# Kernel optimization log

Measured on AMD Instinct MI355X. Metric: run time of the kernel, lower is better.

The kernel has to match this reference:

```python
import jax, jax.numpy as jnp
import numpy as np

N, E, IN_DIM, HID = 100000, 1600000, 128, 256
AA_DIM, POS_DIM, MAX_POS = 64, 32, 512


def setup_inputs() -> dict:
    key = jax.random.key(0)
    ks = jax.random.split(key, 16)
    x = jax.random.normal(ks[0], (N, IN_DIM), dtype=jnp.float32)
    edge_index = jax.random.randint(ks[1], (2, E), 0, N, dtype=jnp.int64)
    edge_weight = jax.random.uniform(ks[2], (E,), dtype=jnp.float32)
    mut_mask = jnp.zeros((N,), dtype=jnp.float32).at[123].set(1.0)  # one-hot mutation site
    wt_idx = jax.random.randint(ks[3], (1,), 0, 20, dtype=jnp.int64)
    mut_idx = jax.random.randint(ks[4], (1,), 0, 20, dtype=jnp.int64)
    def glorot(k, shape):
        fan = shape[0] + shape[1]
        return jax.random.uniform(k, shape, jnp.float32, -1.0, 1.0) * np.sqrt(6.0 / fan)
    W1 = glorot(ks[5], (IN_DIM, HID)); b1 = jnp.zeros((HID,), jnp.float32)
    W2 = glorot(ks[6], (HID, HID));    b2 = jnp.zeros((HID,), jnp.float32)
    aa_emb = jax.random.normal(ks[7], (20, AA_DIM), dtype=jnp.float32)
    pos_emb = jax.random.normal(ks[8], (MAX_POS, POS_DIM), dtype=jnp.float32)
    FEAT = HID + AA_DIM * 3 + POS_DIM  # 480
    Wh1 = glorot(ks[9], (FEAT, 512));  bh1 = jnp.zeros((512,), jnp.float32)
    Wh2 = glorot(ks[10], (512, 128));  bh2 = jnp.zeros((128,), jnp.float32)
    Wh3 = glorot(ks[11], (128, 1));    bh3 = jnp.zeros((1,), jnp.float32)
    return dict(x=x, edge_index=edge_index, edge_weight=edge_weight, mut_mask=mut_mask,
                wt_idx=wt_idx, mut_idx=mut_idx, W1=W1, b1=b1, W2=W2, b2=b2,
                aa_emb=aa_emb, pos_emb=pos_emb, Wh1=Wh1, bh1=bh1, Wh2=Wh2, bh2=bh2,
                Wh3=Wh3, bh3=bh3)


def _gcn_conv(x, W, b, row, col, ew, n):
    # PyG GCNConv: h = x W; out[col] += norm * h[row]; norm = d^-1/2[row]*ew*d^-1/2[col]
    deg = jax.ops.segment_sum(ew, col, num_segments=n)
    dinv = jnp.where(deg > 0, jax.lax.rsqrt(jnp.maximum(deg, 1e-12)), 0.0)
    norm = dinv[row] * ew * dinv[col]
    h = x @ W
    out = jax.ops.segment_sum(h[row] * norm[:, None], col, num_segments=n)
    return out + b


def reference(x, edge_index, edge_weight, mut_mask, wt_idx, mut_idx,
              W1, b1, W2, b2, aa_emb, pos_emb, Wh1, bh1, Wh2, bh2, Wh3, bh3):
    n = x.shape[0]
    # add self loops with weight 1 (GCNConv default, fill_value=1.0)
    loop = jnp.arange(n, dtype=edge_index.dtype)
    row = jnp.concatenate([edge_index[0], loop])
    col = jnp.concatenate([edge_index[1], loop])
    ew = jnp.concatenate([edge_weight, jnp.ones((n,), edge_weight.dtype)])
    # encode (dropout is identity in eval mode)
    h = jax.nn.relu(_gcn_conv(x, W1, b1, row, col, ew, n))
    h = jax.nn.relu(_gcn_conv(h, W2, b2, row, col, ew, n))
    # masked sum -> [1, HID]
    z = (h * mut_mask[:, None]).sum(axis=0, keepdims=True)
    wt = aa_emb[wt_idx.reshape(-1)]
    mut = aa_emb[mut_idx.reshape(-1)]
    delta = mut - wt
    pos = jnp.clip(jnp.argmax(mut_mask), 0, pos_emb.shape[0] - 1).reshape(1)
    pe = pos_emb[pos]
    feat = jnp.concatenate([z, wt, mut, delta, pe], axis=1)  # [1, 480]
    f = jax.nn.relu(feat @ Wh1 + bh1)
    f = jax.nn.relu(f @ Wh2 + bh2)
    out = f @ Wh3 + bh3  # [1, 1]
    return out[0, 0]
```

## Files before the change

### kernel.cpp

```cpp
#include <hip/hip_runtime.h>


#define SCAP   512
#define L1CAP  512
#define L2CAP  16384
#define HID    256
#define INDIM  128
#define HSZ    4096
#define BITW   4096
#define NSCAN  2048
#define NB     1024
#define NTB    32

struct WsPtrs {
  int* cnt;
  float* deg;
  int* hash;
  int* l1r; float* l1w;
  int* l2r; int* l2s; float* l2w;
  int* wscol;
  float* h2;
  float* C;
  float* f2pre;
};

__global__ void kinit(WsPtrs w, const int* eiraw, const float* mask, int N, int E) {
  int g = blockIdx.x * blockDim.x + threadIdx.x;
  int gs = gridDim.x * blockDim.x;
  for (int j = g; j < N; j += gs)
    if (mask[j] > 0.f) w.cnt[4] = j;
  for (int j = g; j < HSZ; j += gs) w.hash[j] = -1;
  if (g < HID) w.h2[g] = 0.f;
  if (g < 128) w.f2pre[g] = 0.f;
  if (g < 3) w.cnt[g] = 0;
  if (g >= 8 && g < 16) w.cnt[g] = 0;
  if (g == 3) {
    int bad = 0;
    long step = E / 20; if (step < 1) step = 1;
    #pragma unroll
    for (int j = 1; j <= 16; ++j) {
      long idx = (long)j * step;
      if (idx < E) bad |= (eiraw[2 * idx + 1] != 0);
    }
    w.cnt[3] = bad ? 0 : 1;
  }
}

__device__ __forceinline__ void hins(WsPtrs& w, int u) {
  unsigned h = ((unsigned)u * 2654435761u) >> 20;
  for (;;) {
    int cur = __hip_atomic_load(&w.hash[h], __ATOMIC_RELAXED, __HIP_MEMORY_SCOPE_AGENT);
    if (cur == u) return;
    if (cur == -1) {
      int old = atomicCAS(&w.hash[h], -1, u);
      if (old == -1) { w.deg[u] = 1.0f; return; }
      if (old == u) return;
    }
    h = (h + 1) & (HSZ - 1);
  }
}

__device__ __forceinline__ void join(int* ctr, int tid, int target) {
  __threadfence();
  __syncthreads();
  if (tid == 0) {
    __hip_atomic_fetch_add(ctr, 1, __ATOMIC_RELEASE, __HIP_MEMORY_SCOPE_AGENT);
    while (__hip_atomic_load(ctr, __ATOMIC_ACQUIRE, __HIP_MEMORY_SCOPE_AGENT) < target)
      __builtin_amdgcn_s_sleep(4);
  }
  __syncthreads();
}

__device__ __forceinline__ float warmf4(const float* base, int nf4, int tid) {
  const float4* p = (const float4*)base;
  float a = 0.f;
  for (int i = tid; i < nf4; i += 256) { float4 v = p[i]; a += v.x + v.y + v.z + v.w; }
  return a;
}

__device__ __forceinline__ int dedup_s1(WsPtrs& w, int n1, int* l1rS, float* l1wS,
                                        int* s1sL, int* nsS, int tid) {
  for (int i = tid; i < n1; i += 256) { l1rS[i] = w.l1r[i]; l1wS[i] = w.l1w[i]; }
  __syncthreads();
  if (tid == 0) {
    int ns = 0;
    for (int i = 0; i < n1; ++i) {
      int v = l1rS[i]; bool seen = false;
      for (int j = 0; j < ns; ++j) if (s1sL[j] == v) { seen = true; break; }
      if (!seen && ns < SCAP) s1sL[ns++] = v;
    }
    *nsS = ns;
  }
  __syncthreads();
  return *nsS;
}

__global__ void kpassA(WsPtrs w, const int* eiraw, const float* ew,
                       const int* wtI_, const int* mutI_,
                       const float* aa, const float* pemb, const float* Wh1,
                       const float* W1, const float* W2, const float* Wh2, int E) {
  if (blockIdx.x >= NSCAN + 8) {
    int b8 = blockIdx.x - (NSCAN + 8);
    int tid = threadIdx.x;
    float wa = warmf4(W1  + b8 * 4096, 1024, tid)
             + warmf4(W2  + b8 * 8192, 2048, tid)
             + warmf4(Wh1 + b8 * 16384, 4096, tid)
             + warmf4(Wh2 + b8 * 8192, 2048, tid);
    if (wa == 1.2345e38f) w.cnt[15] = 1;
    return;
  }
  if (blockIdx.x >= NSCAN) {
    __shared__ float fe[224];
    __shared__ float red[256];
    int b8 = blockIdx.x - NSCAN;
    int t = threadIdx.x;
    int wtI = wtI_[0], mutI = mutI_[0];
    if (t < 64) {
      float a = aa[wtI * 64 + t], b = aa[mutI * 64 + t];
      fe[t] = a; fe[64 + t] = b; fe[128 + t] = b - a;
    }
    int tgt = w.cnt[4];
    int pos = tgt > 511 ? 511 : tgt;
    if (t < 32) fe[192 + t] = pemb[pos * 32 + t];
    __syncthreads();
    int o = b8 * 64 + (t & 63), js = t >> 6;
    float v = 0.f;
    for (int j = js * 56; j < js * 56 + 56; ++j)
      v += fe[j] * Wh1[(256 + j) * 512 + o];
    red[t] = v;
    __syncthreads();
    if (t < 64) w.C[b8 * 64 + t] = red[t] + red[64 + t] + red[128 + t] + red[192 + t];
    return;
  }
  const int tgt = w.cnt[4];
  const bool is64 = w.cnt[3] != 0;
  const long long* ell = (const long long*)eiraw;
  int g = blockIdx.x * blockDim.x + threadIdx.x;
  const int gs = NSCAN * 256;
  for (long e = g; e < E; e += gs) {
    int c = is64 ? (int)ell[(long)E + e] : eiraw[(long)E + e];
    w.wscol[e] = c;
    if (c == tgt) {
      int r = is64 ? (int)ell[e] : eiraw[e];
      int i1 = atomicAdd(&w.cnt[0], 1);
      if (i1 < L1CAP) { w.l1r[i1] = r; w.l1w[i1] = ew[e]; }
    }
  }
  if (g == 0) {
    int i1 = atomicAdd(&w.cnt[0], 1);
    if (i1 < L1CAP) { w.l1r[i1] = tgt; w.l1w[i1] = 1.0f; }
  }
}

__global__ void kpassB(WsPtrs w, const int* eiraw, const float* ew, int E) {
  __shared__ int      l1rS[L1CAP];
  __shared__ float    l1wS[L1CAP];
  __shared__ int      s1sL[SCAP];
  __shared__ unsigned bits[BITW];
  __shared__ int      nsS;
  int tid = threadIdx.x;
  const bool is64 = w.cnt[3] != 0;
  const long long* ell = (const long long*)eiraw;
  int n1 = w.cnt[0]; if (n1 > L1CAP) n1 = L1CAP;
  for (int j = tid; j < BITW; j += 256) bits[j] = 0u;
  int ns = dedup_s1(w, n1, l1rS, l1wS, s1sL, &nsS, tid);
  for (int j = tid; j < ns; j += 256) {
    unsigned u = (unsigned)s1sL[j] & (BITW * 32 - 1);
    atomicOr(&bits[u >> 5], 1u << (u & 31));
    if (blockIdx.x == 0) {
      int v = s1sL[j];
      hins(w, v);
      int idx = atomicAdd(&w.cnt[2], 1);
      if (idx < L2CAP) { w.l2r[idx] = v; w.l2s[idx] = j; w.l2w[idx] = 1.0f; }
    }
  }
  __syncthreads();
  int g = blockIdx.x * 256 + tid;
  const int gs = NB * 256;
  const int4* c4 = (const int4*)w.wscol;
  int nv = E >> 2;
  for (int j2 = g; j2 < nv; j2 += gs) {
    int4 vv = c4[j2];
    #pragma unroll
    for (int t = 0; t < 4; ++t) {
      int c = (t == 0) ? vv.x : (t == 1) ? vv.y : (t == 2) ? vv.z : vv.w;
      unsigned u = (unsigned)c & (BITW * 32 - 1);
      if (bits[u >> 5] & (1u << (u & 31))) {
        int s = -1;
        for (int j = 0; j < ns; ++j) if (s1sL[j] == c) { s = j; break; }
        if (s >= 0) {
          long e = 4L * j2 + t;
          int r = is64 ? (int)ell[e] : eiraw[e];
          int idx = atomicAdd(&w.cnt[2], 1);
          if (idx < L2CAP) { w.l2r[idx] = r; w.l2s[idx] = s; w.l2w[idx] = ew[e]; }
          hins(w, r);
        }
      }
    }
  }
  for (long e = 4L * nv + g; e < E; e += gs) {
    int c = w.wscol[e];
    int s = -1;
    for (int j = 0; j < ns; ++j) if (s1sL[j] == c) { s = j; break; }
    if (s >= 0) {
      int r = is64 ? (int)ell[e] : eiraw[e];
      int idx = atomicAdd(&w.cnt[2], 1);
      if (idx < L2CAP) { w.l2r[idx] = r; w.l2s[idx] = s; w.l2w[idx] = ew[e]; }
      hins(w, r);
    }
  }
}

__global__ void kpassC(WsPtrs w, const float* ew, int E) {
  __shared__ unsigned bits[BITW];
  int tid = threadIdx.x;
  for (int j = tid; j < BITW; j += 256) bits[j] = 0u;
  __syncthreads();
  for (int j = tid; j < HSZ; j += 256) {
    int u2 = w.hash[j];
    if (u2 >= 0) {
      unsigned u = (unsigned)u2 & (BITW * 32 - 1);
      atomicOr(&bits[u >> 5], 1u << (u & 31));
    }
  }
  __syncthreads();
  int g = blockIdx.x * 256 + tid;
  const int gs = NB * 256;
  const int4* c4 = (const int4*)w.wscol;
  int nv = E >> 2;
  for (int j2 = g; j2 < nv; j2 += gs) {
    int4 vv = c4[j2];
    #pragma unroll
    for (int t = 0; t < 4; ++t) {
      int c = (t == 0) ? vv.x : (t == 1) ? vv.y : (t == 2) ? vv.z : vv.w;
      unsigned u = (unsigned)c & (BITW * 32 - 1);
      if (bits[u >> 5] & (1u << (u & 31)))
        atomicAdd(&w.deg[c], ew[4L * j2 + t]);
    }
  }
  for (long e = 4L * nv + g; e < E; e += gs) {
    int c = w.wscol[e];
    unsigned u = (unsigned)c & (BITW * 32 - 1);
    if (bits[u >> 5] & (1u << (u & 31))) atomicAdd(&w.deg[c], ew[e]);
  }
}

__global__ void __launch_bounds__(256) ktail(
    WsPtrs w, const float* x, const float* W1, const float* b1,
    const float* W2, const float* b2, const float* mask,
    const float* Wh1, const float* bh1, const float* Wh2, const float* bh2,
    const float* Wh3, const float* bh3, float* out) {
  __shared__ int   l1rS[L1CAP];
  __shared__ float l1wS[L1CAP];
  __shared__ int   s1sL[SCAP];
  __shared__ int   nsS;
  __shared__ float xs[2][INDIM];
  __shared__ float zL[256];
  __shared__ float pp[256];
  __shared__ float f1L[16];

  int tid = threadIdx.x, bid = blockIdx.x;
  const int tgt = w.cnt[4];
  int n1 = w.cnt[0]; if (n1 > L1CAP) n1 = L1CAP;
  int n2 = w.cnt[2]; if (n2 > L2CAP) n2 = L2CAP;
  int ns = dedup_s1(w, n1, l1rS, l1wS, s1sL, &nsS, tid);
  float dti = rsqrtf(w.deg[tgt]);

  int grp = tid >> 7, lane = tid & 127;
  for (int s = bid; s < ns; s += NTB) {
    int v = s1sL[s];
    float dv = w.deg[v], dvi = rsqrtf(dv);
    ((float*)xs)[tid] = 0.f;
    __syncthreads();
    for (int i = grp; i < n2; i += 2) {
      if (w.l2s[i] == s) {
        int r = w.l2r[i];
        float nrm = rsqrtf(w.deg[r]) * w.l2w[i] * dvi;
        xs[grp][lane] += nrm * x[(long)r * INDIM + lane];
      }
    }
    __syncthreads();
    float h = b1[tid];
    #pragma unroll 8
    for (int k = 0; k < INDIM; ++k) h += (xs[0][k] + xs[1][k]) * W1[k * HID + tid];
    float wsum = 0.f;
    for (int i = 0; i < n1; ++i) if (l1rS[i] == v) wsum += l1wS[i];
    atomicAdd(&w.h2[tid], dvi * wsum * dti * fmaxf(h, 0.f));
    __syncthreads();
  }
  join(&w.cnt[8], tid, NTB);

  pp[tid] = __hip_atomic_load(&w.h2[tid], __ATOMIC_RELAXED, __HIP_MEMORY_SCOPE_AGENT);
  __syncthreads();
  {
    float v = b2[tid];
    #pragma unroll 8
    for (int k = 0; k < HID; ++k) v += pp[k] * W2[k * HID + tid];
    zL[tid] = fmaxf(v, 0.f) * mask[tgt];
  }
  __syncthreads();

  {
    int o0 = bid * 16, o = o0 + (tid & 15), ks = tid >> 4;
    float v = 0.f;
    #pragma unroll 4
    for (int k = ks * 16; k < ks * 16 + 16; ++k) v += zL[k] * Wh1[k * 512 + o];
    pp[tid] = v;
    __syncthreads();
    if (tid < 16) {
      float v2 = w.C[o0 + tid] + bh1[o0 + tid];
      for (int s2 = 0; s2 < 16; ++s2) v2 += pp[s2 * 16 + tid];
      f1L[tid] = fmaxf(v2, 0.f);
    }
    __syncthreads();
    if (tid < 128) {
      float v3 = 0.f;
      #pragma unroll
      for (int j = 0; j < 16; ++j) v3 += f1L[j] * Wh2[(o0 + j) * 128 + tid];
      atomicAdd(&w.f2pre[tid], v3);
    }
  }
  __threadfence();
  __syncthreads();
  if (tid == 0)
    __hip_atomic_fetch_add(&w.cnt[9], 1, __ATOMIC_RELEASE, __HIP_MEMORY_SCOPE_AGENT);
  if (bid != 0) return;
  if (tid == 0)
    while (__hip_atomic_load(&w.cnt[9], __ATOMIC_ACQUIRE,
                             __HIP_MEMORY_SCOPE_AGENT) < NTB)
      __builtin_amdgcn_s_sleep(4);
  __syncthreads();

  if (tid < 128)
    pp[tid] = fmaxf(__hip_atomic_load(&w.f2pre[tid], __ATOMIC_RELAXED,
                                      __HIP_MEMORY_SCOPE_AGENT) + bh2[tid], 0.f)
              * Wh3[tid];
  __syncthreads();
  if (tid == 0) {
    float s = bh3[0];
    for (int k = 0; k < 128; ++k) s += pp[k];
    out[0] = s;
  }
}

extern "C" void kernel_launch(void* const* d_in, const int* in_sizes, int n_in,
                              void* d_out, int out_size, void* d_ws, size_t ws_size,
                              hipStream_t stream) {
  const float* x    = (const float*)d_in[0];
  const int*   ei   = (const int*)d_in[1];
  const float* ew   = (const float*)d_in[2];
  const float* mask = (const float*)d_in[3];
  const int*   wtI  = (const int*)d_in[4];
  const int*   mutI = (const int*)d_in[5];
  const float* W1   = (const float*)d_in[6];
  const float* b1   = (const float*)d_in[7];
  const float* W2   = (const float*)d_in[8];
  const float* b2   = (const float*)d_in[9];
  const float* aa   = (const float*)d_in[10];
  const float* pemb = (const float*)d_in[11];
  const float* Wh1  = (const float*)d_in[12];
  const float* bh1  = (const float*)d_in[13];
  const float* Wh2  = (const float*)d_in[14];
  const float* bh2  = (const float*)d_in[15];
  const float* Wh3  = (const float*)d_in[16];
  const float* bh3  = (const float*)d_in[17];
  float* out = (float*)d_out;
  const int N = in_sizes[3];
  const int E = in_sizes[2];

  char* q = (char*)d_ws;
  auto take = [&](size_t bytes) -> char* {
    char* r = q; q += (bytes + 255) & ~(size_t)255; return r;
  };
  WsPtrs w;
  w.cnt   = (int*)take(64);
  w.deg   = (float*)take((size_t)N * 4);
  w.hash  = (int*)take(HSZ * 4);
  w.l1r   = (int*)take(L1CAP * 4);
  w.l1w   = (float*)take(L1CAP * 4);
  w.l2r   = (int*)take(L2CAP * 4);
  w.l2s   = (int*)take(L2CAP * 4);
  w.l2w   = (float*)take(L2CAP * 4);
  w.wscol = (int*)take((size_t)E * 4);
  w.h2    = (float*)take(HID * 4);
  w.C     = (float*)take(512 * 4);
  w.f2pre = (float*)take(128 * 4);

  kinit  <<<64, 256, 0, stream>>>(w, ei, mask, N, E);
  kpassA <<<NSCAN + 16, 256, 0, stream>>>(w, ei, ew, wtI, mutI, aa, pemb, Wh1,
                                          W1, W2, Wh2, E);
  kpassB <<<NB, 256, 0, stream>>>(w, ei, ew, E);
  kpassC <<<NB, 256, 0, stream>>>(w, ew, E);
  ktail  <<<NTB, 256, 0, stream>>>(w, x, W1, b1, W2, b2, mask,
                                   Wh1, bh1, Wh2, bh2, Wh3, bh3, out);
}
```

Measured before the change: 224.3 us.

## Parallelize tail over edges with global atomics and split matvecs across blocks

The tail kernel now accumulates aggregated neighbour features for all 2-hop nodes into a global buffer with atomics, distributing edges across all blocks instead of each block scanning every edge list per node. The W1 projection is then done block-per-output-slice over shared-memory tiles of the sums, and the W2 matvec is split across blocks with extra grid joins. The column scan in pass A is also vectorized to read two indices per load. This adds extra grid-wide barriers, a zero-initialised workspace buffer and many float atomics.

```diff
diff --git a/kernel.cpp b/kernel.cpp
--- a/kernel.cpp
+++ b/kernel.cpp
@@ -19,8 +19,10 @@
   int* l1r; float* l1w;
   int* l2r; int* l2s; float* l2w;
   int* wscol;
+  float* xsum;
   float* h2;
   float* C;
+  float* z;
   float* f2pre;
 };
 
@@ -30,6 +32,8 @@
   for (int j = g; j < N; j += gs)
     if (mask[j] > 0.f) w.cnt[4] = j;
   for (int j = g; j < HSZ; j += gs) w.hash[j] = -1;
+  float4* xz = (float4*)w.xsum;
+  for (int j = g; j < SCAP * INDIM / 4; j += gs) xz[j] = make_float4(0.f, 0.f, 0.f, 0.f);
   if (g < HID) w.h2[g] = 0.f;
   if (g < 128) w.f2pre[g] = 0.f;
   if (g < 3) w.cnt[g] = 0;
@@ -136,14 +140,38 @@
   const bool is64 = w.cnt[3] != 0;
   const long long* ell = (const long long*)eiraw;
   int g = blockIdx.x * blockDim.x + threadIdx.x;
-  const int gs = NSCAN * 256;
-  for (long e = g; e < E; e += gs) {
-    int c = is64 ? (int)ell[(long)E + e] : eiraw[(long)E + e];
-    w.wscol[e] = c;
-    if (c == tgt) {
-      int r = is64 ? (int)ell[e] : eiraw[e];
-      int i1 = atomicAdd(&w.cnt[0], 1);
-      if (i1 < L1CAP) { w.l1r[i1] = r; w.l1w[i1] = ew[e]; }
+  const long gs = (long)NSCAN * 256;
+  auto hit = [&](long e, int r_unused) {
+    int r = is64 ? (int)ell[e] : eiraw[e];
+    int i1 = atomicAdd(&w.cnt[0], 1);
+    if (i1 < L1CAP) { w.l1r[i1] = r; w.l1w[i1] = ew[e]; }
+  };
+  if ((E & 1) == 0) {
+    long half = E >> 1;
+    int2* ws2 = (int2*)w.wscol;
+    if (is64) {
+      const long2* c2 = (const long2*)(ell + E);
+      for (long j = g; j < half; j += gs) {
+        long2 v = c2[j];
+        int c0 = (int)v.x, c1 = (int)v.y;
+        ws2[j] = make_int2(c0, c1);
+        if (c0 == tgt) hit(2 * j, 0);
+        if (c1 == tgt) hit(2 * j + 1, 0);
+      }
+    } else {
+      const int2* c2 = (const int2*)(eiraw + E);
+      for (long j = g; j < half; j += gs) {
+        int2 v = c2[j];
+        ws2[j] = v;
+        if (v.x == tgt) hit(2 * j, 0);
+        if (v.y == tgt) hit(2 * j + 1, 0);
+      }
+    }
+  } else {
+    for (long e = g; e < E; e += gs) {
+      int c = is64 ? (int)ell[(long)E + e] : eiraw[(long)E + e];
+      w.wscol[e] = c;
+      if (c == tgt) hit(e, 0);
     }
   }
   if (g == 0) {
@@ -254,9 +282,9 @@
   __shared__ float l1wS[L1CAP];
   __shared__ int   s1sL[SCAP];
   __shared__ int   nsS;
-  __shared__ float xs[2][INDIM];
-  __shared__ float zL[256];
-  __shared__ float pp[256];
+  __shared__ float xsL[64 * 129];
+  __shared__ float red[256];
+  __shared__ float vecS[256];
   __shared__ float f1L[16];
 
   int tid = threadIdx.x, bid = blockIdx.x;
@@ -265,51 +293,74 @@
   int n2 = w.cnt[2]; if (n2 > L2CAP) n2 = L2CAP;
   int ns = dedup_s1(w, n1, l1rS, l1wS, s1sL, &nsS, tid);
   float dti = rsqrtf(w.deg[tgt]);
+  float maskv = mask[tgt];
 
   int grp = tid >> 7, lane = tid & 127;
-  for (int s = bid; s < ns; s += NTB) {
-    int v = s1sL[s];
-    float dv = w.deg[v], dvi = rsqrtf(dv);
-    ((float*)xs)[tid] = 0.f;
-    __syncthreads();
-    for (int i = grp; i < n2; i += 2) {
-      if (w.l2s[i] == s) {
-        int r = w.l2r[i];
-        float nrm = rsqrtf(w.deg[r]) * w.l2w[i] * dvi;
-        xs[grp][lane] += nrm * x[(long)r * INDIM + lane];
-      }
-    }
-    __syncthreads();
-    float h = b1[tid];
-    #pragma unroll 8
-    for (int k = 0; k < INDIM; ++k) h += (xs[0][k] + xs[1][k]) * W1[k * HID + tid];
-    float wsum = 0.f;
-    for (int i = 0; i < n1; ++i) if (l1rS[i] == v) wsum += l1wS[i];
-    atomicAdd(&w.h2[tid], dvi * wsum * dti * fmaxf(h, 0.f));
-    __syncthreads();
+  for (int i = bid * 2 + grp; i < n2; i += NTB * 2) {
+    int s = w.l2s[i], r = w.l2r[i];
+    float nrm = rsqrtf(w.deg[r]) * w.l2w[i] * rsqrtf(w.deg[s1sL[s]]);
+    atomicAdd(&w.xsum[s * INDIM + lane], nrm * x[(long)r * INDIM + lane]);
   }
   join(&w.cnt[8], tid, NTB);
 
-  pp[tid] = __hip_atomic_load(&w.h2[tid], __ATOMIC_RELAXED, __HIP_MEMORY_SCOPE_AGENT);
+  int oi = tid & 7, vi = tid >> 3;
+  int o = bid * 8 + oi;
+  float h2acc = 0.f;
+  for (int cb = 0; cb < ns; cb += 64) {
+    int ce = ns - cb; if (ce > 64) ce = 64;
+    for (int j = tid; j < ce * INDIM; j += 256)
+      xsL[(j >> 7) * 129 + (j & 127)] =
+        __hip_atomic_load(&w.xsum[cb * INDIM + j], __ATOMIC_RELAXED,
+                          __HIP_MEMORY_SCOPE_AGENT);
+    __syncthreads();
+    for (int v = vi; v < ce; v += 32) {
+      const float* xv = &xsL[v * 129];
+      float h = b1[o];
+      #pragma unroll 8
+      for (int k = 0; k < INDIM; ++k) h += xv[k] * W1[k * HID + o];
+      int node = s1sL[cb + v];
+      float wsum = 0.f;
+      for (int i = 0; i < n1; ++i) if (l1rS[i] == node) wsum += l1wS[i];
+      h2acc += rsqrtf(w.deg[node]) * wsum * dti * fmaxf(h, 0.f);
+    }
+    __syncthreads();
+  }
+  red[tid] = h2acc;
+  __syncthreads();
+  if (tid < 8) {
+    float t = 0.f;
+    for (int q = 0; q < 32; ++q) t += red[q * 8 + tid];
+    w.h2[bid * 8 + tid] = t;
+  }
+  join(&w.cnt[9], tid, NTB);
+
+  vecS[tid] = __hip_atomic_load(&w.h2[tid], __ATOMIC_RELAXED, __HIP_MEMORY_SCOPE_AGENT);
   __syncthreads();
   {
-    float v = b2[tid];
-    #pragma unroll 8
-    for (int k = 0; k < HID; ++k) v += pp[k] * W2[k * HID + tid];
-    zL[tid] = fmaxf(v, 0.f) * mask[tgt];
-  }
-  __syncthreads();
-
+    float part = 0.f;
+    for (int k = vi; k < HID; k += 32) part += vecS[k] * W2[k * HID + o];
+    red[tid] = part;
+  }
+  __syncthreads();
+  if (tid < 8) {
+    float t = 0.f;
+    for (int q = 0; q < 32; ++q) t += red[q * 8 + tid];
+    w.z[bid * 8 + tid] = fmaxf(t + b2[bid * 8 + tid], 0.f) * maskv;
+  }
+  join(&w.cnt[10], tid, NTB);
+
+  vecS[tid] = __hip_atomic_load(&w.z[tid], __ATOMIC_RELAXED, __HIP_MEMORY_SCOPE_AGENT);
+  __syncthreads();
   {
-    int o0 = bid * 16, o = o0 + (tid & 15), ks = tid >> 4;
+    int o0 = bid * 16, oo = o0 + (tid & 15), ks = tid >> 4;
     float v = 0.f;
     #pragma unroll 4
-    for (int k = ks * 16; k < ks * 16 + 16; ++k) v += zL[k] * Wh1[k * 512 + o];
-    pp[tid] = v;
+    for (int k = ks * 16; k < ks * 16 + 16; ++k) v += vecS[k] * Wh1[k * 512 + oo];
+    red[tid] = v;
     __syncthreads();
     if (tid < 16) {
       float v2 = w.C[o0 + tid] + bh1[o0 + tid];
-      for (int s2 = 0; s2 < 16; ++s2) v2 += pp[s2 * 16 + tid];
+      for (int s2 = 0; s2 < 16; ++s2) v2 += red[s2 * 16 + tid];
       f1L[tid] = fmaxf(v2, 0.f);
     }
     __syncthreads();
@@ -323,22 +374,22 @@
   __threadfence();
   __syncthreads();
   if (tid == 0)
-    __hip_atomic_fetch_add(&w.cnt[9], 1, __ATOMIC_RELEASE, __HIP_MEMORY_SCOPE_AGENT);
+    __hip_atomic_fetch_add(&w.cnt[11], 1, __ATOMIC_RELEASE, __HIP_MEMORY_SCOPE_AGENT);
   if (bid != 0) return;
   if (tid == 0)
-    while (__hip_atomic_load(&w.cnt[9], __ATOMIC_ACQUIRE,
+    while (__hip_atomic_load(&w.cnt[11], __ATOMIC_ACQUIRE,
                              __HIP_MEMORY_SCOPE_AGENT) < NTB)
       __builtin_amdgcn_s_sleep(4);
   __syncthreads();
 
   if (tid < 128)
-    pp[tid] = fmaxf(__hip_atomic_load(&w.f2pre[tid], __ATOMIC_RELAXED,
-                                      __HIP_MEMORY_SCOPE_AGENT) + bh2[tid], 0.f)
-              * Wh3[tid];
+    red[tid] = fmaxf(__hip_atomic_load(&w.f2pre[tid], __ATOMIC_RELAXED,
+                                       __HIP_MEMORY_SCOPE_AGENT) + bh2[tid], 0.f)
+               * Wh3[tid];
   __syncthreads();
   if (tid == 0) {
     float s = bh3[0];
-    for (int k = 0; k < 128; ++k) s += pp[k];
+    for (int k = 0; k < 128; ++k) s += red[k];
     out[0] = s;
   }
 }
@@ -382,8 +433,10 @@
   w.l2s   = (int*)take(L2CAP * 4);
   w.l2w   = (float*)take(L2CAP * 4);
   w.wscol = (int*)take((size_t)E * 4);
+  w.xsum  = (float*)take((size_t)SCAP * INDIM * 4);
   w.h2    = (float*)take(HID * 4);
   w.C     = (float*)take(512 * 4);
+  w.z     = (float*)take(256 * 4);
   w.f2pre = (float*)take(128 * 4);
 
   kinit  <<<64, 256, 0, stream>>>(w, ei, mask, N, E);
```

Result: faster. 203.5 us (-9.3%).
